# Kernel optimization log

Hardware: AMD Instinct MI355X
Metric: run time of the kernel (lower is better)

Reference implementation:

```python
import jax, jax.numpy as jnp
import numpy as np

VOCAB = 100000
EMB = 100
HID = 100
CTX_LEN = 60          # must equal MAX_DESC_LEN for linear_1 to fit
FACT_LEN = 20
DESC_LEN = 60


def setup_inputs() -> dict:
    key = jax.random.key(0)
    ks = jax.random.split(key, 12)
    s = 0.05
    context = jax.random.randint(ks[0], (CTX_LEN, FACT_LEN), 1, VOCAB)
    fact_lengths = jax.random.randint(ks[1], (CTX_LEN,), 1, FACT_LEN)
    description = jax.random.randint(ks[2], (DESC_LEN,), 1, VOCAB)
    emb_ctx = jax.random.normal(ks[3], (VOCAB, EMB), jnp.float32) * s
    emb_ctx = emb_ctx.at[0].set(0.0)  # padding_idx=0
    emb_dec = jax.random.normal(ks[4], (VOCAB, EMB), jnp.float32) * s
    emb_dec = emb_dec.at[0].set(0.0)
    w1 = jax.random.normal(ks[5], (HID, CTX_LEN * HID), jnp.float32) * s
    b1 = jax.random.normal(ks[6], (HID,), jnp.float32) * s
    w_ih = jax.random.normal(ks[7], (3 * HID, EMB), jnp.float32) * s
    w_hh = jax.random.normal(ks[8], (3 * HID, HID), jnp.float32) * s
    b_ih = jax.random.normal(ks[9], (3 * HID,), jnp.float32) * s
    b_hh = jax.random.normal(ks[10], (3 * HID,), jnp.float32) * s
    w_out = jax.random.normal(ks[11], (VOCAB, HID), jnp.float32) * s
    b_out = jnp.zeros((VOCAB,), jnp.float32)
    return {"context": context, "fact_lengths": fact_lengths, "description": description,
            "emb_ctx": emb_ctx, "emb_dec": emb_dec, "w1": w1, "b1": b1,
            "w_ih": w_ih, "w_hh": w_hh, "b_ih": b_ih, "b_hh": b_hh,
            "w_out": w_out, "b_out": b_out}


def _forward(context, description, emb_ctx, emb_dec, w1, b1,
             w_ih, w_hh, b_ih, b_hh, w_out, b_out):
    # ---- InputModule: embed + positional fact encoder ----
    emb = emb_ctx[context]                       # [CTX_LEN, FACT_LEN, EMB]
    slen, elen = FACT_LEN, EMB
    s = jnp.arange(slen, dtype=jnp.float32) / (slen - 1)   # [slen]
    e = jnp.arange(elen, dtype=jnp.float32) / (elen - 1)   # [elen]
    l = 1.0 - s[:, None] - e[None, :] * (1.0 - 2.0 * s[:, None])  # [slen, elen]
    facts = jnp.sum(emb * l[None], axis=1)       # [CTX_LEN, EMB]

    # ---- initial decoder hidden from flattened facts ----
    h0 = facts.reshape(1, -1) @ w1.T + b1        # [1, HID]

    x0 = emb_dec[1][None, :]                     # SOS token embedding [1, EMB]

    def step(carry, tok):
        h, x = carry
        gi = x @ w_ih.T + b_ih                   # [1, 3H]
        gh = h @ w_hh.T + b_hh
        i_r, i_z, i_n = jnp.split(gi, 3, axis=-1)
        h_r, h_z, h_n = jnp.split(gh, 3, axis=-1)
        r = jax.nn.sigmoid(i_r + h_r)
        z = jax.nn.sigmoid(i_z + h_z)
        n = jnp.tanh(i_n + r * h_n)
        h_new = (1.0 - z) * n + z * h            # [1, HID]
        logits = h_new @ w_out.T + b_out         # [1, VOCAB]
        logp = jax.nn.log_softmax(logits, axis=-1)
        loss_t = -logp[0, tok]                   # NLLLoss, batch 1
        x_next = emb_dec[tok][None, :]           # teacher forcing
        return (h_new, x_next), loss_t

    (_, _), losses = jax.lax.scan(step, (h0, x0), description)
    return jnp.sum(losses).reshape(1)            # matches torch FloatTensor([.])


def reference(context, fact_lengths, description, emb_ctx, emb_dec, w1, b1,
              w_ih, w_hh, b_ih, b_hh, w_out, b_out):
    # fact_lengths is unused by the original forward (PositionalFactEncoder ignores it)
    return _forward(context, description, emb_ctx, emb_dec, w1, b1,
                    w_ih, w_hh, b_ih, b_hh, w_out, b_out)
```

## Files before the change

kernel.cpp:

```cpp
#include <hip/hip_runtime.h>
#include <hip/hip_bf16.h>
#include <math.h>

#define VOCAB 100000
#define EMB 100
#define HID 100
#define CTX_LEN 60
#define FACT_LEN 20
#define DESC_LEN 60
#define NCHUNK (VOCAB / 16)

#define WS_FACTS 0
#define WS_X     6000
#define WS_H0    12000
#define WS_GI    12160
#define WS_H     30160
#define WS_MS    36864

typedef __attribute__((ext_vector_type(8))) short short8;
typedef __attribute__((ext_vector_type(4))) float f32x4;

static __device__ __forceinline__ unsigned short f2bf(float f) {
    union { float f; unsigned u; } x; x.f = f;
    unsigned r = (x.u + 0x7FFFu + ((x.u >> 16) & 1u)) >> 16;
    return (unsigned short)r;
}

__global__ __launch_bounds__(128) void k1_prep(const int* __restrict__ context,
                                               const int* __restrict__ desc,
                                               const float* __restrict__ emb_ctx,
                                               const float* __restrict__ emb_dec,
                                               float* __restrict__ ws,
                                               float* __restrict__ out) {
    int b = blockIdx.x, tid = threadIdx.x;
    if (b < 60) {
        __shared__ int toks[20];
        if (tid < 20) toks[tid] = context[b * 20 + tid];
        __syncthreads();
        if (tid < 100) {
            float ef = tid * (1.f / 99.f);
            float acc = 0.f;
            #pragma unroll
            for (int s = 0; s < 20; s++) {
                float sf = s * (1.f / 19.f);
                float l = 1.f - sf - ef * (1.f - 2.f * sf);
                acc = fmaf(emb_ctx[toks[s] * 100 + tid], l, acc);
            }
            ws[WS_FACTS + b * 100 + tid] = acc;
        }
    } else {
        int t = b - 60;
        int tok = (t == 0) ? 1 : desc[t - 1];
        if (tid < 100) ws[WS_X + t * 100 + tid] = emb_dec[tok * 100 + tid];
        if (b == 60 && tid == 0) out[0] = 0.f;
    }
}

__global__ __launch_bounds__(320) void k2_h0_gi(const float* __restrict__ w1,
                                                const float* __restrict__ b1,
                                                const float* __restrict__ w_ih,
                                                const float* __restrict__ b_ih,
                                                float* __restrict__ ws) {
    int b = blockIdx.x, tid = threadIdx.x;
    if (b < 100) {
        __shared__ float red[320];
        const float* facts = ws + WS_FACTS;
        const float* wr = w1 + b * 6000;
        float p = 0.f;
        for (int k = tid; k < 6000; k += 320) p = fmaf(facts[k], wr[k], p);
        red[tid] = p; __syncthreads();
        if (tid < 64) red[tid] += red[256 + tid];
        __syncthreads();
        for (int st = 128; st > 0; st >>= 1) {
            if (tid < st) red[tid] += red[tid + st];
            __syncthreads();
        }
        if (tid == 0) ws[WS_H0 + b] = red[0] + b1[b];
    } else {
        int t = b - 100;
        __shared__ float xs[100];
        if (tid < 100) xs[tid] = ws[WS_X + t * 100 + tid];
        __syncthreads();
        if (tid < 300) {
            float p = b_ih[tid];
            const float* wr = w_ih + tid * 100;
            #pragma unroll 4
            for (int k = 0; k < 100; k++) p = fmaf(wr[k], xs[k], p);
            ws[WS_GI + t * 300 + tid] = p;
        }
    }
}

__global__ __launch_bounds__(320, 1) void k3_gru(const float* __restrict__ w_hh,
                                                 const float* __restrict__ b_hh,
                                                 float* __restrict__ ws) {
    __shared__ __align__(16) float h_lds[128];
    __shared__ float gh_lds[304];
    const int j = threadIdx.x;
    float wreg[100];
    float bhh = 0.f;
    if (j < 300) {
        bhh = b_hh[j];
        #pragma unroll
        for (int k4 = 0; k4 < 25; k4++) {
            float4 v = *(const float4*)(w_hh + j * 100 + k4 * 4);
            wreg[k4 * 4 + 0] = v.x; wreg[k4 * 4 + 1] = v.y;
            wreg[k4 * 4 + 2] = v.z; wreg[k4 * 4 + 3] = v.w;
        }
    }
    float hreg = 0.f;
    if (j < 100) { hreg = ws[WS_H0 + j]; h_lds[j] = hreg; }
    __syncthreads();

    const float* gi = ws + WS_GI;
    float* H = ws + WS_H;
    for (int t = 0; t < 60; t++) {
        if (j < 300) {
            float a0 = bhh, a1 = 0.f, a2 = 0.f, a3 = 0.f;
            #pragma unroll
            for (int k4 = 0; k4 < 25; k4++) {
                float4 hv = *(const float4*)(h_lds + k4 * 4);
                a0 = fmaf(wreg[k4 * 4 + 0], hv.x, a0);
                a1 = fmaf(wreg[k4 * 4 + 1], hv.y, a1);
                a2 = fmaf(wreg[k4 * 4 + 2], hv.z, a2);
                a3 = fmaf(wreg[k4 * 4 + 3], hv.w, a3);
            }
            gh_lds[j] = (a0 + a1) + (a2 + a3);
        }
        __syncthreads();
        if (j < 100) {
            float gir = gi[t * 300 + j];
            float giz = gi[t * 300 + 100 + j];
            float gin = gi[t * 300 + 200 + j];
            float ghr = gh_lds[j], ghz = gh_lds[100 + j], ghn = gh_lds[200 + j];
            float r = 1.f / (1.f + __expf(-(gir + ghr)));
            float z = 1.f / (1.f + __expf(-(giz + ghz)));
            float a = fmaf(r, ghn, gin);
            float tt = __expf(-2.f * fabsf(a));
            float n = copysignf((1.f - tt) / (1.f + tt), a);
            hreg = (1.f - z) * n + z * hreg;
            h_lds[j] = hreg;
            H[t * 100 + j] = hreg;
        }
        __syncthreads();
    }
}

__global__ __launch_bounds__(256, 1) void k4_logits(const float* __restrict__ w_out,
                                                    const float* __restrict__ b_out,
                                                    float* __restrict__ ws,
                                                    int nwaves) {
    const float* H = ws + WS_H;
    float* ms = ws + WS_MS;
    const int lane = threadIdx.x & 63;
    const int gw = blockIdx.x * 4 + (threadIdx.x >> 6);
    const int q = lane >> 4, n = lane & 15;
    const int k_base = q * 8;

    short8 afr[4][4];
    #pragma unroll
    for (int mt = 0; mt < 4; mt++) {
        int m = mt * 16 + n;
        #pragma unroll
        for (int kt = 0; kt < 4; kt++) {
            int k0 = kt * 32 + k_base;
            float va[8];
            #pragma unroll
            for (int jj = 0; jj < 8; jj++) va[jj] = 0.f;
            if (m < 60) {
                if (k0 + 4 <= 100) {
                    float4 a = *(const float4*)(H + m * 100 + k0);
                    va[0] = a.x; va[1] = a.y; va[2] = a.z; va[3] = a.w;
                }
                if (k0 + 8 <= 100) {
                    float4 b = *(const float4*)(H + m * 100 + k0 + 4);
                    va[4] = b.x; va[5] = b.y; va[6] = b.z; va[7] = b.w;
                }
            }
            short8 f;
            #pragma unroll
            for (int jj = 0; jj < 8; jj++) f[jj] = (short)f2bf(va[jj]);
            afr[mt][kt] = f;
        }
    }

    float mS[16], sS[16];
    #pragma unroll
    for (int i = 0; i < 16; i++) { mS[i] = -3.0e38f; sS[i] = 0.f; }

    for (int c = gw; c < NCHUNK; c += nwaves) {
        int row = c * 16 + n;
        short8 bfr[4];
        #pragma unroll
        for (int kt = 0; kt < 4; kt++) {
            int k0 = kt * 32 + k_base;
            float va[8];
            #pragma unroll
            for (int jj = 0; jj < 8; jj++) va[jj] = 0.f;
            if (k0 + 4 <= 100) {
                float4 a = *(const float4*)(w_out + row * 100 + k0);
                va[0] = a.x; va[1] = a.y; va[2] = a.z; va[3] = a.w;
            }
            if (k0 + 8 <= 100) {
                float4 b = *(const float4*)(w_out + row * 100 + k0 + 4);
                va[4] = b.x; va[5] = b.y; va[6] = b.z; va[7] = b.w;
            }
            short8 f;
            #pragma unroll
            for (int jj = 0; jj < 8; jj++) f[jj] = (short)f2bf(va[jj]);
            bfr[kt] = f;
        }
        float bo = b_out[row];
        #pragma unroll
        for (int mt = 0; mt < 4; mt++) {
            f32x4 acc = {0.f, 0.f, 0.f, 0.f};
            acc = __builtin_amdgcn_mfma_f32_16x16x32_bf16(afr[mt][0], bfr[0], acc, 0, 0, 0);
            acc = __builtin_amdgcn_mfma_f32_16x16x32_bf16(afr[mt][1], bfr[1], acc, 0, 0, 0);
            acc = __builtin_amdgcn_mfma_f32_16x16x32_bf16(afr[mt][2], bfr[2], acc, 0, 0, 0);
            acc = __builtin_amdgcn_mfma_f32_16x16x32_bf16(afr[mt][3], bfr[3], acc, 0, 0, 0);
            #pragma unroll
            for (int reg = 0; reg < 4; reg++) {
                float x = acc[reg] + bo;
                int i = mt * 4 + reg;
                float mo = mS[i];
                float mn = fmaxf(mo, x);
                sS[i] = sS[i] * __expf(mo - mn) + __expf(x - mn);
                mS[i] = mn;
            }
        }
    }

    #pragma unroll
    for (int i = 0; i < 16; i++) {
        float m = mS[i], s = sS[i];
        #pragma unroll
        for (int off = 1; off < 16; off <<= 1) {
            float m2 = __shfl_xor(m, off);
            float s2 = __shfl_xor(s, off);
            float mn = fmaxf(m, m2);
            s = s * __expf(m - mn) + s2 * __expf(m2 - mn);
            m = mn;
        }
        mS[i] = m; sS[i] = s;
    }
    if (n == 0) {
        #pragma unroll
        for (int mt = 0; mt < 4; mt++) {
            #pragma unroll
            for (int reg = 0; reg < 4; reg++) {
                int t = mt * 16 + q * 4 + reg;
                int i = mt * 4 + reg;
                if (t < 60) {
                    float2 val; val.x = mS[i]; val.y = sS[i];
                    ((float2*)ms)[t * nwaves + gw] = val;
                }
            }
        }
    }
}

__global__ __launch_bounds__(256) void k5_final(const int* __restrict__ desc,
                                                const float* __restrict__ w_out,
                                                const float* __restrict__ b_out,
                                                const float* __restrict__ ws,
                                                float* __restrict__ out,
                                                int nwaves) {
    int t = blockIdx.x, tid = threadIdx.x;
    __shared__ float sm[256], ss[256], sd[256];
    const float2* ms = (const float2*)(ws + WS_MS);
    float m = -3.0e38f, s = 0.f;
    for (int i = tid; i < nwaves; i += 256) {
        float2 p = ms[t * nwaves + i];
        float mn = fmaxf(m, p.x);
        s = s * __expf(m - mn) + p.y * __expf(p.x - mn);
        m = mn;
    }
    sm[tid] = m; ss[tid] = s; __syncthreads();
    for (int st = 128; st > 0; st >>= 1) {
        if (tid < st) {
            float mo = sm[tid], so = ss[tid];
            float m2 = sm[tid + st], s2 = ss[tid + st];
            float mn = fmaxf(mo, m2);
            sm[tid] = mn;
            ss[tid] = so * __expf(mo - mn) + s2 * __expf(m2 - mn);
        }
        __syncthreads();
    }
    int tok = desc[t];
    float p = 0.f;
    if (tid < 100) p = ws[WS_H + t * 100 + tid] * w_out[tok * 100 + tid];
    sd[tid] = p; __syncthreads();
    for (int st = 128; st > 0; st >>= 1) {
        if (tid < st) sd[tid] += sd[tid + st];
        __syncthreads();
    }
    if (tid == 0) {
        float logit = sd[0] + b_out[tok];
        float loss = sm[0] + logf(ss[0]) - logit;
        atomicAdd(out, loss);
    }
}

extern "C" void kernel_launch(void* const* d_in, const int* in_sizes, int n_in,
                              void* d_out, int out_size, void* d_ws, size_t ws_size,
                              hipStream_t stream) {
    const int*   context = (const int*)d_in[0];
    const int*   desc    = (const int*)d_in[2];
    const float* emb_ctx = (const float*)d_in[3];
    const float* emb_dec = (const float*)d_in[4];
    const float* w1      = (const float*)d_in[5];
    const float* b1      = (const float*)d_in[6];
    const float* w_ih    = (const float*)d_in[7];
    const float* w_hh    = (const float*)d_in[8];
    const float* b_ih    = (const float*)d_in[9];
    const float* b_hh    = (const float*)d_in[10];
    const float* w_out   = (const float*)d_in[11];
    const float* b_out   = (const float*)d_in[12];
    float* out = (float*)d_out;
    float* ws  = (float*)d_ws;

    int nblocks = 512;
    size_t need = (size_t)(WS_MS + 60 * (nblocks * 4) * 2) * 4;
    if (ws_size < need) nblocks = 256;
    int nwaves = nblocks * 4;

    k1_prep  <<<120, 128, 0, stream>>>(context, desc, emb_ctx, emb_dec, ws, out);
    k2_h0_gi <<<160, 320, 0, stream>>>(w1, b1, w_ih, b_ih, ws);
    k3_gru   <<<1,   320, 0, stream>>>(w_hh, b_hh, ws);
    k4_logits<<<nblocks, 256, 0, stream>>>(w_out, b_out, ws, nwaves);
    k5_final <<<60,  256, 0, stream>>>(desc, w_out, b_out, ws, out, nwaves);
}
```

Before: 248.1 us.

## Run GRU recurrent matvec on bf16 MFMA, stage gates in LDS, fix logits grid

The sequential GRU kernel now keeps w_hh as bf16 MFMA B-fragments in registers. Each step's h·W_hh product runs as 16x16x32 bf16 MFMAs instead of 100 scalar FMAs per thread. All precomputed input-gate values are copied into shared memory up front, so no global loads sit on the per-step critical path. The logits kernel is also fixed at 256 blocks with a compile-time wave count, which drops the 512-block path. The risks are bf16 rounding of the hidden state and weights compounding over 60 steps, and the halved logits grid.

```diff
diff --git a/kernel.cpp b/kernel.cpp
--- a/kernel.cpp
+++ b/kernel.cpp
@@ -9,6 +9,7 @@
 #define FACT_LEN 20
 #define DESC_LEN 60
 #define NCHUNK (VOCAB / 16)
+#define NWAVES 1024
 
 #define WS_FACTS 0
 #define WS_X     6000
@@ -94,53 +95,85 @@
 __global__ __launch_bounds__(320, 1) void k3_gru(const float* __restrict__ w_hh,
                                                  const float* __restrict__ b_hh,
                                                  float* __restrict__ ws) {
-    __shared__ __align__(16) float h_lds[128];
-    __shared__ float gh_lds[304];
-    const int j = threadIdx.x;
-    float wreg[100];
-    float bhh = 0.f;
-    if (j < 300) {
-        bhh = b_hh[j];
-        #pragma unroll
-        for (int k4 = 0; k4 < 25; k4++) {
-            float4 v = *(const float4*)(w_hh + j * 100 + k4 * 4);
-            wreg[k4 * 4 + 0] = v.x; wreg[k4 * 4 + 1] = v.y;
-            wreg[k4 * 4 + 2] = v.z; wreg[k4 * 4 + 3] = v.w;
-        }
-    }
-    float hreg = 0.f;
-    if (j < 100) { hreg = ws[WS_H0 + j]; h_lds[j] = hreg; }
+    __shared__ float gi_lds[18000];
+    __shared__ float gh_lds[320];
+    __shared__ __align__(16) unsigned short h_bf[128];
+
+    const int tid = threadIdx.x;
+    const int wave = tid >> 6, lane = tid & 63;
+    const int q = lane >> 4, n = lane & 15;
+
+    short8 bfr[16];
+    #pragma unroll
+    for (int i = 0; i < 4; i++) {
+        int row = (wave * 4 + i) * 16 + n;
+        const float* wr = w_hh + row * 100;
+        #pragma unroll
+        for (int kt = 0; kt < 4; kt++) {
+            int k0 = kt * 32 + q * 8;
+            float va[8];
+            #pragma unroll
+            for (int jj = 0; jj < 8; jj++) va[jj] = 0.f;
+            if (row < 300) {
+                if (k0 + 4 <= 100) {
+                    float4 a = *(const float4*)(wr + k0);
+                    va[0] = a.x; va[1] = a.y; va[2] = a.z; va[3] = a.w;
+                }
+                if (k0 + 8 <= 100) {
+                    float4 b = *(const float4*)(wr + k0 + 4);
+                    va[4] = b.x; va[5] = b.y; va[6] = b.z; va[7] = b.w;
+                }
+            }
+            short8 f;
+            #pragma unroll
+            for (int jj = 0; jj < 8; jj++) f[jj] = (short)f2bf(va[jj]);
+            bfr[i * 4 + kt] = f;
+        }
+    }
+
+    for (int k = tid; k < 18000; k += 320) gi_lds[k] = ws[WS_GI + k];
+
+    float hreg = 0.f, bh0 = 0.f, bh1 = 0.f, bh2 = 0.f;
+    if (tid < 100) {
+        hreg = ws[WS_H0 + tid];
+        h_bf[tid] = f2bf(hreg);
+        bh0 = b_hh[tid]; bh1 = b_hh[100 + tid]; bh2 = b_hh[200 + tid];
+    } else if (tid < 128) {
+        h_bf[tid] = 0;
+    }
     __syncthreads();
 
-    const float* gi = ws + WS_GI;
     float* H = ws + WS_H;
     for (int t = 0; t < 60; t++) {
-        if (j < 300) {
-            float a0 = bhh, a1 = 0.f, a2 = 0.f, a3 = 0.f;
-            #pragma unroll
-            for (int k4 = 0; k4 < 25; k4++) {
-                float4 hv = *(const float4*)(h_lds + k4 * 4);
-                a0 = fmaf(wreg[k4 * 4 + 0], hv.x, a0);
-                a1 = fmaf(wreg[k4 * 4 + 1], hv.y, a1);
-                a2 = fmaf(wreg[k4 * 4 + 2], hv.z, a2);
-                a3 = fmaf(wreg[k4 * 4 + 3], hv.w, a3);
-            }
-            gh_lds[j] = (a0 + a1) + (a2 + a3);
-        }
-        __syncthreads();
-        if (j < 100) {
-            float gir = gi[t * 300 + j];
-            float giz = gi[t * 300 + 100 + j];
-            float gin = gi[t * 300 + 200 + j];
-            float ghr = gh_lds[j], ghz = gh_lds[100 + j], ghn = gh_lds[200 + j];
+        short8 afr[4];
+        #pragma unroll
+        for (int kt = 0; kt < 4; kt++)
+            afr[kt] = *(const short8*)&h_bf[kt * 32 + q * 8];
+        #pragma unroll
+        for (int i = 0; i < 4; i++) {
+            f32x4 a = {0.f, 0.f, 0.f, 0.f};
+            a = __builtin_amdgcn_mfma_f32_16x16x32_bf16(afr[0], bfr[i * 4 + 0], a, 0, 0, 0);
+            a = __builtin_amdgcn_mfma_f32_16x16x32_bf16(afr[1], bfr[i * 4 + 1], a, 0, 0, 0);
+            a = __builtin_amdgcn_mfma_f32_16x16x32_bf16(afr[2], bfr[i * 4 + 2], a, 0, 0, 0);
+            a = __builtin_amdgcn_mfma_f32_16x16x32_bf16(afr[3], bfr[i * 4 + 3], a, 0, 0, 0);
+            if (lane < 16) gh_lds[(wave * 4 + i) * 16 + lane] = a[0];
+        }
+        __syncthreads();
+        if (tid < 100) {
+            float gir = gi_lds[t * 300 + tid];
+            float giz = gi_lds[t * 300 + 100 + tid];
+            float gin = gi_lds[t * 300 + 200 + tid];
+            float ghr = gh_lds[tid] + bh0;
+            float ghz = gh_lds[100 + tid] + bh1;
+            float ghn = gh_lds[200 + tid] + bh2;
             float r = 1.f / (1.f + __expf(-(gir + ghr)));
             float z = 1.f / (1.f + __expf(-(giz + ghz)));
             float a = fmaf(r, ghn, gin);
             float tt = __expf(-2.f * fabsf(a));
-            float n = copysignf((1.f - tt) / (1.f + tt), a);
-            hreg = (1.f - z) * n + z * hreg;
-            h_lds[j] = hreg;
-            H[t * 100 + j] = hreg;
+            float nn = copysignf((1.f - tt) / (1.f + tt), a);
+            hreg = (1.f - z) * nn + z * hreg;
+            h_bf[tid] = f2bf(hreg);
+            H[t * 100 + tid] = hreg;
         }
         __syncthreads();
     }
@@ -148,8 +181,7 @@
 
 __global__ __launch_bounds__(256, 1) void k4_logits(const float* __restrict__ w_out,
                                                     const float* __restrict__ b_out,
-                                                    float* __restrict__ ws,
-                                                    int nwaves) {
+                                                    float* __restrict__ ws) {
     const float* H = ws + WS_H;
     float* ms = ws + WS_MS;
     const int lane = threadIdx.x & 63;
@@ -188,7 +220,7 @@
     #pragma unroll
     for (int i = 0; i < 16; i++) { mS[i] = -3.0e38f; sS[i] = 0.f; }
 
-    for (int c = gw; c < NCHUNK; c += nwaves) {
+    for (int c = gw; c < NCHUNK; c += NWAVES) {
         int row = c * 16 + n;
         short8 bfr[4];
         #pragma unroll
@@ -252,7 +284,7 @@
                 int i = mt * 4 + reg;
                 if (t < 60) {
                     float2 val; val.x = mS[i]; val.y = sS[i];
-                    ((float2*)ms)[t * nwaves + gw] = val;
+                    ((float2*)ms)[t * NWAVES + gw] = val;
                 }
             }
         }
@@ -263,14 +295,13 @@
                                                 const float* __restrict__ w_out,
                                                 const float* __restrict__ b_out,
                                                 const float* __restrict__ ws,
-                                                float* __restrict__ out,
-                                                int nwaves) {
+                                                float* __restrict__ out) {
     int t = blockIdx.x, tid = threadIdx.x;
     __shared__ float sm[256], ss[256], sd[256];
     const float2* ms = (const float2*)(ws + WS_MS);
     float m = -3.0e38f, s = 0.f;
-    for (int i = tid; i < nwaves; i += 256) {
-        float2 p = ms[t * nwaves + i];
+    for (int i = tid; i < NWAVES; i += 256) {
+        float2 p = ms[t * NWAVES + i];
         float mn = fmaxf(m, p.x);
         s = s * __expf(m - mn) + p.y * __expf(p.x - mn);
         m = mn;
@@ -319,14 +350,9 @@
     float* out = (float*)d_out;
     float* ws  = (float*)d_ws;
 
-    int nblocks = 512;
-    size_t need = (size_t)(WS_MS + 60 * (nblocks * 4) * 2) * 4;
-    if (ws_size < need) nblocks = 256;
-    int nwaves = nblocks * 4;
-
     k1_prep  <<<120, 128, 0, stream>>>(context, desc, emb_ctx, emb_dec, ws, out);
     k2_h0_gi <<<160, 320, 0, stream>>>(w1, b1, w_ih, b_ih, ws);
     k3_gru   <<<1,   320, 0, stream>>>(w_hh, b_hh, ws);
-    k4_logits<<<nblocks, 256, 0, stream>>>(w_out, b_out, ws, nwaves);
-    k5_final <<<60,  256, 0, stream>>>(desc, w_out, b_out, ws, out, nwaves);
-}
+    k4_logits<<<256, 256, 0, stream>>>(w_out, b_out, ws);
+    k5_final <<<60,  256, 0, stream>>>(desc, w_out, b_out, ws, out);
+}
```

Result: faster. 204.0 us (-17.8%).
